# Performance work log

Hardware: AMD Instinct MI355X
Metric: run time of the kernel (lower is better)

Reference implementation:

```python
import jax, jax.numpy as jnp
import numpy as np

N_NODES = 4096        # number of sum nodes in this layer
N_CHILD = 16384       # total number of child-layer nodes
DEGREE = 64           # fan-in per sum node
NNZ = N_NODES * DEGREE
BATCH = 128


def setup_inputs() -> dict:
    key = jax.random.key(0)
    k1, k2, k3 = jax.random.split(key, 3)
    child_ll = jax.random.normal(k1, (BATCH, N_CHILD), dtype=jnp.float32)
    log_w = jax.random.normal(k2, (NNZ,), dtype=jnp.float32)
    # each sum node has exactly DEGREE incoming edges (sorted segment ids)
    rows = jnp.repeat(jnp.arange(N_NODES, dtype=jnp.int32), DEGREE)
    cols = jax.random.randint(k3, (NNZ,), 0, N_CHILD, dtype=jnp.int32)
    return {"child_ll": child_ll, "log_w": log_w, "rows": rows, "cols": cols}


def _segment_logsumexp(v, seg, num_segments):
    # v: [E, ...], seg: [E] -> [num_segments, ...], numerically stable
    m = jax.ops.segment_max(v, seg, num_segments=num_segments)
    m = jax.lax.stop_gradient(m)
    s = jax.ops.segment_sum(jnp.exp(v - m[seg]), seg, num_segments=num_segments)
    return m + jnp.log(s)


def reference(child_ll, log_w, rows, cols):
    # per-edge weighted child log-likelihood: [E, B]
    v = child_ll.T[cols] + log_w[:, None]
    # unnormalized sum-node log-likelihood: [N, B]
    ll = _segment_logsumexp(v, rows, N_NODES)
    # per-node log normalization constant logsumexp(log_w) over each row: [N]
    log_z = _segment_logsumexp(log_w, rows, N_NODES)
    return (ll - log_z[:, None]).T  # [B, N]
```

## Files before the change

kernel.cpp:

```cpp
#include <hip/hip_runtime.h>
#include <hip/hip_bf16.h>

#define N_NODES 4096
#define N_CHILD 16384
#define DEGREE  64
#define BATCH   128

__global__ __launch_bounds__(256)
void exp_transpose_kernel(const float* __restrict__ in,
                          __hip_bfloat16* __restrict__ out) {
    __shared__ float tile[32][33];
    const int c0 = blockIdx.x * 32;
    const int b0 = blockIdx.y * 32;
    const int tx = threadIdx.x;
    const int ty = threadIdx.y;
#pragma unroll
    for (int j = 0; j < 32; j += 8)
        tile[ty + j][tx] = __expf(in[(size_t)(b0 + ty + j) * N_CHILD + (c0 + tx)]);
    __syncthreads();
#pragma unroll
    for (int j = 0; j < 32; j += 8)
        out[(size_t)(c0 + ty + j) * BATCH + (b0 + tx)] =
            __float2bfloat16(tile[tx][ty + j]);
}

__global__ __launch_bounds__(256)
void sum_layer_kernel(const __hip_bfloat16* __restrict__ childE,
                      const float* __restrict__ log_w,
                      const int*   __restrict__ cols,
                      float* __restrict__ outT)
{
    const int tid  = threadIdx.x;
    const int wave = __builtin_amdgcn_readfirstlane(tid >> 6);
    const int lane = tid & 63;
    const int n    = blockIdx.x * 4 + wave;
    const int e0   = n * DEGREE;

    const float w  = log_w[e0 + lane];
    const float ew = __expf(w);
    float sw = ew;
#pragma unroll
    for (int off = 32; off >= 1; off >>= 1)
        sw += __shfl_xor(sw, off);
    const float lz = __logf(sw);

    const unsigned int* __restrict__ rowE = (const unsigned int*)childE;

    float s0 = 0.0f, s1 = 0.0f;
#pragma unroll
    for (int d = 0; d < DEGREE; ++d) {
        const int   c   = cols[e0 + d];
        const float ewd = __shfl(ew, d);
        const unsigned int u = rowE[c * 64 + lane];
        const float f0 = __uint_as_float(u << 16);
        const float f1 = __uint_as_float(u & 0xffff0000u);
        s0 = fmaf(f0, ewd, s0);
        s1 = fmaf(f1, ewd, s1);
    }

    float2 r;
    r.x = __logf(s0) - lz;
    r.y = __logf(s1) - lz;
    ((float2*)(outT + (size_t)n * BATCH))[lane] = r;
}

__global__ __launch_bounds__(256)
void transpose_kernel(const float* __restrict__ in, float* __restrict__ out,
                      int R, int C) {
    __shared__ float tile[32][33];
    const int c0 = blockIdx.x * 32;
    const int r0 = blockIdx.y * 32;
    const int tx = threadIdx.x;
    const int ty = threadIdx.y;
#pragma unroll
    for (int j = 0; j < 32; j += 8)
        tile[ty + j][tx] = in[(size_t)(r0 + ty + j) * C + (c0 + tx)];
    __syncthreads();
#pragma unroll
    for (int j = 0; j < 32; j += 8)
        out[(size_t)(c0 + ty + j) * R + (r0 + tx)] = tile[tx][ty + j];
}

extern "C" void kernel_launch(void* const* d_in, const int* in_sizes, int n_in,
                              void* d_out, int out_size, void* d_ws, size_t ws_size,
                              hipStream_t stream) {
    const float* child_ll = (const float*)d_in[0];
    const float* log_w    = (const float*)d_in[1];
    const int*   cols     = (const int*)d_in[3];
    float*       out      = (float*)d_out;

    __hip_bfloat16* childE = (__hip_bfloat16*)d_ws;
    float* outT = (float*)((char*)d_ws + (size_t)N_CHILD * BATCH * 2);

    {
        dim3 tb(32, 8), tg(N_CHILD / 32, BATCH / 32);
        exp_transpose_kernel<<<tg, tb, 0, stream>>>(child_ll, childE);
    }

    sum_layer_kernel<<<N_NODES / 4, 256, 0, stream>>>(childE, log_w, cols, outT);

    {
        dim3 tb(32, 8), tg(BATCH / 32, N_NODES / 32);
        transpose_kernel<<<tg, tb, 0, stream>>>(outT, out, N_NODES, BATCH);
    }
}
```

Baseline: 74.89 us.

## Fuse output transpose into sum-layer kernel via shared-memory staging

Removes the separate transpose kernel by having each block compute 8 sum nodes (2 per wave), stage the results in shared memory, and write the [B,N] output directly. This saves one launch and the round trip of the intermediate through global memory. The inner loop also uses two independent accumulator pairs so more loads can be in flight. The output writes are 32-byte segments per batch row rather than fully coalesced, and the block now needs a sync.

Measured after the change: 75.50 us. No clear change (+0.8%).

```diff
diff --git a/kernel.cpp b/kernel.cpp
--- a/kernel.cpp
+++ b/kernel.cpp
@@ -5,6 +5,7 @@
 #define N_CHILD 16384
 #define DEGREE  64
 #define BATCH   128
+#define NT      8
 
 __global__ __launch_bounds__(256)
 void exp_transpose_kernel(const float* __restrict__ in,
@@ -28,57 +29,59 @@
 void sum_layer_kernel(const __hip_bfloat16* __restrict__ childE,
                       const float* __restrict__ log_w,
                       const int*   __restrict__ cols,
-                      float* __restrict__ outT)
+                      float* __restrict__ out)
 {
     const int tid  = threadIdx.x;
     const int wave = __builtin_amdgcn_readfirstlane(tid >> 6);
     const int lane = tid & 63;
-    const int n    = blockIdx.x * 4 + wave;
-    const int e0   = n * DEGREE;
+    const int n0   = blockIdx.x * NT;
 
-    const float w  = log_w[e0 + lane];
-    const float ew = __expf(w);
-    float sw = ew;
-#pragma unroll
-    for (int off = 32; off >= 1; off >>= 1)
-        sw += __shfl_xor(sw, off);
-    const float lz = __logf(sw);
+    __shared__ float res[NT][130];
 
     const unsigned int* __restrict__ rowE = (const unsigned int*)childE;
 
-    float s0 = 0.0f, s1 = 0.0f;
 #pragma unroll
-    for (int d = 0; d < DEGREE; ++d) {
-        const int   c   = cols[e0 + d];
-        const float ewd = __shfl(ew, d);
-        const unsigned int u = rowE[c * 64 + lane];
-        const float f0 = __uint_as_float(u << 16);
-        const float f1 = __uint_as_float(u & 0xffff0000u);
-        s0 = fmaf(f0, ewd, s0);
-        s1 = fmaf(f1, ewd, s1);
+    for (int t = 0; t < 2; ++t) {
+        const int jl = wave * 2 + t;
+        const int e0 = (n0 + jl) * DEGREE;
+
+        const float ew = __expf(log_w[e0 + lane]);
+        float sw = ew;
+#pragma unroll
+        for (int off = 32; off >= 1; off >>= 1)
+            sw += __shfl_xor(sw, off);
+        const float lz = __logf(sw);
+
+        float s0a = 0.f, s0b = 0.f, s1a = 0.f, s1b = 0.f;
+#pragma unroll
+        for (int d = 0; d < DEGREE; d += 2) {
+            const int ca = cols[e0 + d];
+            const int cb = cols[e0 + d + 1];
+            const float ewa = __shfl(ew, d);
+            const float ewb = __shfl(ew, d + 1);
+            const unsigned int ua = rowE[ca * 64 + lane];
+            const unsigned int ub = rowE[cb * 64 + lane];
+            s0a = fmaf(__uint_as_float(ua << 16),          ewa, s0a);
+            s1a = fmaf(__uint_as_float(ua & 0xffff0000u),  ewa, s1a);
+            s0b = fmaf(__uint_as_float(ub << 16),          ewb, s0b);
+            s1b = fmaf(__uint_as_float(ub & 0xffff0000u),  ewb, s1b);
+        }
+
+        float2 r;
+        r.x = __logf(s0a + s0b) - lz;
+        r.y = __logf(s1a + s1b) - lz;
+        *(float2*)&res[jl][2 * lane] = r;
     }
 
-    float2 r;
-    r.x = __logf(s0) - lz;
-    r.y = __logf(s1) - lz;
-    ((float2*)(outT + (size_t)n * BATCH))[lane] = r;
-}
+    __syncthreads();
 
-__global__ __launch_bounds__(256)
-void transpose_kernel(const float* __restrict__ in, float* __restrict__ out,
-                      int R, int C) {
-    __shared__ float tile[32][33];
-    const int c0 = blockIdx.x * 32;
-    const int r0 = blockIdx.y * 32;
-    const int tx = threadIdx.x;
-    const int ty = threadIdx.y;
 #pragma unroll
-    for (int j = 0; j < 32; j += 8)
-        tile[ty + j][tx] = in[(size_t)(r0 + ty + j) * C + (c0 + tx)];
-    __syncthreads();
-#pragma unroll
-    for (int j = 0; j < 32; j += 8)
-        out[(size_t)(c0 + ty + j) * R + (r0 + tx)] = tile[tx][ty + j];
+    for (int p = 0; p < 4; ++p) {
+        const int idx = p * 256 + tid;
+        const int j = idx & (NT - 1);
+        const int b = idx >> 3;
+        out[(size_t)b * N_NODES + n0 + j] = res[j][b];
+    }
 }
 
 extern "C" void kernel_launch(void* const* d_in, const int* in_sizes, int n_in,
@@ -90,17 +93,11 @@
     float*       out      = (float*)d_out;
 
     __hip_bfloat16* childE = (__hip_bfloat16*)d_ws;
-    float* outT = (float*)((char*)d_ws + (size_t)N_CHILD * BATCH * 2);
 
     {
         dim3 tb(32, 8), tg(N_CHILD / 32, BATCH / 32);
         exp_transpose_kernel<<<tg, tb, 0, stream>>>(child_ll, childE);
     }
 
-    sum_layer_kernel<<<N_NODES / 4, 256, 0, stream>>>(childE, log_w, cols, outT);
-
-    {
-        dim3 tb(32, 8), tg(BATCH / 32, N_NODES / 32);
-        transpose_kernel<<<tg, tb, 0, stream>>>(outT, out, N_NODES, BATCH);
-    }
+    sum_layer_kernel<<<N_NODES / NT, 256, 0, stream>>>(childE, log_w, cols, out);
 }
```
